# Performance work log

Hardware: AMD Instinct MI355X
Metric: run time of the kernel (lower is better)

## Reference

```python
import math
import jax, jax.numpy as jnp
import numpy as np

N_HEADS = 16
D_EMBED = 1024
D_HEAD = D_EMBED // N_HEADS
BATCH = 2
SEQ = 2048


def setup_inputs() -> dict:
    key = jax.random.key(0)
    k1, k2, k3 = jax.random.split(key, 3)
    scale = 1.0 / math.sqrt(D_EMBED)
    return {
        "x": jax.random.normal(k1, (1, BATCH, SEQ, D_EMBED), dtype=jnp.float32),
        "w_in": jax.random.normal(k2, (3 * D_EMBED, D_EMBED), dtype=jnp.float32) * scale,
        "b_in": jnp.zeros((3 * D_EMBED,), dtype=jnp.float32),
        "w_out": jax.random.normal(k3, (D_EMBED, D_EMBED), dtype=jnp.float32) * scale,
        "b_out": jnp.zeros((D_EMBED,), dtype=jnp.float32),
        "causal_mask": 1,
    }


def reference(x, w_in, b_in, w_out, b_out, causal_mask):
    lead, B, S, D = x.shape  # lead == 1
    H, dh = N_HEADS, D_HEAD
    # fused QKV projection (torch Linear: x @ W^T + b)
    qkv = jnp.einsum("lbsd,ed->lbse", x, w_in) + b_in
    q, k, v = jnp.split(qkv, 3, axis=-1)
    # [1,B,S,D] -> [B,H,S,dh]
    def to_heads(t):
        return t.reshape(B, S, H, dh).transpose(0, 2, 1, 3)
    q, k, v = to_heads(q), to_heads(k), to_heads(v)
    # scaled dot-product attention with optional causal mask
    scores = jnp.einsum("bhqd,bhkd->bhqk", q, k)
    if causal_mask:
        mask = jnp.triu(jnp.ones((S, S), dtype=bool), k=1)
        scores = jnp.where(mask, -jnp.inf, scores)
    scores = scores / math.sqrt(dh)
    attn = jax.nn.softmax(scores, axis=-1)
    out = jnp.einsum("bhqk,bhkd->bhqd", attn, v)
    out = out.transpose(0, 2, 1, 3).reshape(lead, B, S, D)
    return jnp.einsum("lbsd,ed->lbse", out, w_out) + b_out
```

## Files before the change

### kernel.cpp

```cpp
#include <hip/hip_runtime.h>
#include <hip/hip_bf16.h>
#include <stdint.h>

#define S_LEN 2048
#define D_EMB 1024
#define NHEAD 16
#define DHEAD 64
#define NBATCH 2
#define MROWS 4096

typedef __attribute__((ext_vector_type(8))) short bf16x8;
typedef __attribute__((ext_vector_type(4))) float f32x4;
typedef unsigned short u16;
typedef unsigned int u32;

__device__ __forceinline__ u16 f2bf(float f) {
  union { float f; u32 u; } v; v.f = f;
  u32 r = v.u + 0x7fffu + ((v.u >> 16) & 1u);
  return (u16)(r >> 16);
}

__device__ __forceinline__ void gl_lds16(const void* g, void* l) {
  __builtin_amdgcn_global_load_lds(
      (const __attribute__((address_space(1))) u32*)g,
      (__attribute__((address_space(3))) u32*)l, 16, 0, 0);
}

__device__ __forceinline__ int swz(int o) { return o ^ (((o >> 7) & 7) << 4); }

__global__ void cast_f32_bf16(const float* __restrict__ in, u16* __restrict__ out, int n4) {
  int i = blockIdx.x * blockDim.x + threadIdx.x;
  if (i < n4) {
    float4 v = reinterpret_cast<const float4*>(in)[i];
    ushort4 o;
    o.x = f2bf(v.x); o.y = f2bf(v.y); o.z = f2bf(v.z); o.w = f2bf(v.w);
    reinterpret_cast<ushort4*>(out)[i] = o;
  }
}

template <int EPI>
__launch_bounds__(256, 2)
__global__ void gemm_bt(const u16* __restrict__ A, const u16* __restrict__ Bm,
                        const float* __restrict__ bias, int M, int N, int K,
                        u16* __restrict__ q_out, u16* __restrict__ k_out,
                        u16* __restrict__ vt_out, float* __restrict__ f_out) {
  __shared__ __align__(16) u16 As[2][128 * 32];
  __shared__ __align__(16) u16 Bs[2][128 * 32];
  const int t = threadIdx.x;
  const int w = t >> 6, lane = t & 63;
  const int m0 = blockIdx.y * 128, n0 = blockIdx.x * 128;
  const int wr = w >> 1, wc = w & 1;

  f32x4 acc[4][4] = {};

  const int e0 = w * 512 + lane * 8;
  const int ar0 = e0 >> 5, ac0 = e0 & 31;
  const int e1 = e0 + 2048;
  const int ar1 = e1 >> 5, ac1 = e1 & 31;
  const u16* Ab0 = A + (size_t)(m0 + ar0) * K + ac0;
  const u16* Ab1 = A + (size_t)(m0 + ar1) * K + ac1;
  const u16* Bb0 = Bm + (size_t)(n0 + ar0) * K + ac0;
  const u16* Bb1 = Bm + (size_t)(n0 + ar1) * K + ac1;

  const int lr = lane & 15, lg = lane >> 4;

#define GSTAGE(KT, BUF)                                \
  do {                                                 \
    gl_lds16(Ab0 + (KT), &As[BUF][w * 512]);           \
    gl_lds16(Ab1 + (KT), &As[BUF][w * 512 + 2048]);    \
    gl_lds16(Bb0 + (KT), &Bs[BUF][w * 512]);           \
    gl_lds16(Bb1 + (KT), &Bs[BUF][w * 512 + 2048]);    \
  } while (0)

  GSTAGE(0, 0);
  __syncthreads();
  int cur = 0;
  for (int kt = 0; kt < K; kt += 32) {
    if (kt + 32 < K) GSTAGE(kt + 32, cur ^ 1);
    bf16x8 af[4], bfr[4];
#pragma unroll
    for (int i = 0; i < 4; i++)
      af[i] = *(const bf16x8*)&As[cur][(wr * 64 + i * 16 + lr) * 32 + lg * 8];
#pragma unroll
    for (int j = 0; j < 4; j++)
      bfr[j] = *(const bf16x8*)&Bs[cur][(wc * 64 + j * 16 + lr) * 32 + lg * 8];
#pragma unroll
    for (int i = 0; i < 4; i++)
#pragma unroll
      for (int j = 0; j < 4; j++)
        acc[i][j] = __builtin_amdgcn_mfma_f32_16x16x32_bf16(af[i], bfr[j], acc[i][j], 0, 0, 0);
    __syncthreads();
    cur ^= 1;
  }
#undef GSTAGE

#pragma unroll
  for (int j = 0; j < 4; j++) {
    const int n = n0 + wc * 64 + j * 16 + lr;
    const float bv = bias[n];
#pragma unroll
    for (int i = 0; i < 4; i++) {
#pragma unroll
      for (int r = 0; r < 4; r++) {
        const int m = m0 + wr * 64 + i * 16 + lg * 4 + r;
        float v = acc[i][j][r] + bv;
        if (EPI == 0) {
          const int which = n >> 10, nn = n & 1023;
          const int h = nn >> 6, d = nn & 63;
          const int b = m >> 11, s = m & 2047;
          if (which == 0)
            q_out[(size_t)(((b * NHEAD + h) * S_LEN) + s) * DHEAD + d] = f2bf(v * 0.125f);
          else if (which == 1)
            k_out[(size_t)(((b * NHEAD + h) * S_LEN) + s) * DHEAD + d] = f2bf(v);
          else
            vt_out[(size_t)(((b * NHEAD + h) * DHEAD) + d) * S_LEN + s] = f2bf(v);
        } else {
          f_out[(size_t)m * N + n] = v;
        }
      }
    }
  }
}

__launch_bounds__(512, 2)
__global__ void attn_kernel(const u16* __restrict__ Qg, const u16* __restrict__ Kg,
                            const u16* __restrict__ Vtg, u16* __restrict__ AO,
                            const int* __restrict__ causal) {
  __shared__ __align__(16) u16 Kt[2][64 * 64];
  __shared__ __align__(16) u16 Vt[2][64 * 64];
  __shared__ __align__(16) u16 Pl[8][16 * 72];

  const int t = threadIdx.x, w = t >> 6, lane = t & 63;
  const int lr = lane & 15, lg = lane >> 4;
  const int qt = (int)(gridDim.x - 1) - (int)blockIdx.x;
  const int bh = blockIdx.y;
  const size_t bh_off = (size_t)bh * S_LEN * DHEAD;
  const int cz = *causal;
  const int q0 = qt * 128;
  const int nk = cz ? (2 * qt + 2) : (S_LEN / 64);

  {
    const char* qb = (const char*)(Qg + bh_off + (size_t)q0 * DHEAD);
#pragma unroll
    for (int c = 0; c < 2; c++) {
      int drel = c * 8192 + w * 1024 + lane * 16;
      gl_lds16(qb + swz(drel), (char*)&Kt[0][0] + c * 8192 + w * 1024);
    }
  }
  __syncthreads();
  bf16x8 qf[2];
#pragma unroll
  for (int ks = 0; ks < 2; ks++) {
    int rq = w * 16 + lr;
    qf[ks] = *(const bf16x8*)((const char*)&Kt[0][0] + swz(rq * 128 + ks * 64 + lg * 16));
  }
  __syncthreads();

  auto stageK = [&](int kt, int buf) {
    const char* kb = (const char*)(Kg + bh_off + (size_t)kt * 64 * DHEAD);
    int drel = w * 1024 + lane * 16;
    gl_lds16(kb + swz(drel), (char*)&Kt[buf][0] + w * 1024);
  };
  auto stageV = [&](int kt, int buf) {
    int drel = w * 1024 + lane * 16;
    int o = swz(drel);
    int row = o >> 7, colb = o & 127;
    const char* vb = (const char*)Vtg +
                     (((size_t)bh * DHEAD + row) * S_LEN + (size_t)kt * 64) * 2 + colb;
    gl_lds16(vb, (char*)&Vt[buf][0] + w * 1024);
  };

  float m_run[4], l_run[4];
  f32x4 o_acc[4] = {};
#pragma unroll
  for (int r = 0; r < 4; r++) { m_run[r] = -INFINITY; l_run[r] = 0.f; }

  stageK(0, 0);
  stageV(0, 0);
  __syncthreads();
  int cur = 0;

  for (int kt = 0; kt < nk; kt++) {
    if (kt + 1 < nk) {
      stageK(kt + 1, cur ^ 1);
      stageV(kt + 1, cur ^ 1);
    }

    f32x4 s[4] = {};
#pragma unroll
    for (int nf = 0; nf < 4; nf++) {
#pragma unroll
      for (int ks = 0; ks < 2; ks++) {
        int r = nf * 16 + lr;
        bf16x8 kf = *(const bf16x8*)((const char*)&Kt[cur][0] + swz(r * 128 + ks * 64 + lg * 16));
        s[nf] = __builtin_amdgcn_mfma_f32_16x16x32_bf16(qf[ks], kf, s[nf], 0, 0, 0);
      }
    }

    if (cz && (kt * 64 + 63 > q0 + w * 16)) {
#pragma unroll
      for (int nf = 0; nf < 4; nf++)
#pragma unroll
        for (int r = 0; r < 4; r++) {
          int kv = kt * 64 + nf * 16 + lr;
          int qr = q0 + w * 16 + lg * 4 + r;
          if (kv > qr) s[nf][r] = -INFINITY;
        }
    }

    float rmax[4];
#pragma unroll
    for (int r = 0; r < 4; r++) {
      rmax[r] = s[0][r];
#pragma unroll
      for (int nf = 1; nf < 4; nf++) rmax[r] = fmaxf(rmax[r], s[nf][r]);
    }
#pragma unroll
    for (int mlt = 1; mlt < 16; mlt <<= 1)
#pragma unroll
      for (int r = 0; r < 4; r++) rmax[r] = fmaxf(rmax[r], __shfl_xor(rmax[r], mlt, 64));

    float scl[4];
#pragma unroll
    for (int r = 0; r < 4; r++) {
      float mn = fmaxf(m_run[r], rmax[r]);
      scl[r] = __expf(m_run[r] - mn);
      m_run[r] = mn;
    }

    float rsum[4] = {0.f, 0.f, 0.f, 0.f};
#pragma unroll
    for (int nf = 0; nf < 4; nf++)
#pragma unroll
      for (int r = 0; r < 4; r++) {
        float p = __expf(s[nf][r] - m_run[r]);
        rsum[r] += p;
        Pl[w][(lg * 4 + r) * 72 + nf * 16 + lr] = f2bf(p);
      }
#pragma unroll
    for (int mlt = 1; mlt < 16; mlt <<= 1)
#pragma unroll
      for (int r = 0; r < 4; r++) rsum[r] += __shfl_xor(rsum[r], mlt, 64);
#pragma unroll
    for (int r = 0; r < 4; r++) l_run[r] = l_run[r] * scl[r] + rsum[r];
#pragma unroll
    for (int nf = 0; nf < 4; nf++)
#pragma unroll
      for (int r = 0; r < 4; r++) o_acc[nf][r] *= scl[r];

    asm volatile("s_waitcnt lgkmcnt(0)" ::: "memory");
    __builtin_amdgcn_sched_barrier(0);

    bf16x8 pf[2];
#pragma unroll
    for (int ks = 0; ks < 2; ks++)
      pf[ks] = *(const bf16x8*)&Pl[w][lr * 72 + ks * 32 + lg * 8];
#pragma unroll
    for (int nf = 0; nf < 4; nf++) {
#pragma unroll
      for (int ks = 0; ks < 2; ks++) {
        int r = nf * 16 + lr;
        bf16x8 vf = *(const bf16x8*)((const char*)&Vt[cur][0] + swz(r * 128 + ks * 64 + lg * 16));
        o_acc[nf] = __builtin_amdgcn_mfma_f32_16x16x32_bf16(pf[ks], vf, o_acc[nf], 0, 0, 0);
      }
    }

    __syncthreads();
    cur ^= 1;
  }

  const int b = bh >> 4, h = bh & 15;
#pragma unroll
  for (int nf = 0; nf < 4; nf++)
#pragma unroll
    for (int r = 0; r < 4; r++) {
      float v = o_acc[nf][r] / l_run[r];
      int qrow = q0 + w * 16 + lg * 4 + r;
      int d = nf * 16 + lr;
      AO[(size_t)(b * S_LEN + qrow) * D_EMB + h * DHEAD + d] = f2bf(v);
    }
}

extern "C" void kernel_launch(void* const* d_in, const int* in_sizes, int n_in,
                              void* d_out, int out_size, void* d_ws, size_t ws_size,
                              hipStream_t stream) {
  const float* x = (const float*)d_in[0];
  const float* w_in = (const float*)d_in[1];
  const float* b_in = (const float*)d_in[2];
  const float* w_out = (const float*)d_in[3];
  const float* b_out = (const float*)d_in[4];
  const int* causal = (const int*)d_in[5];
  float* out = (float*)d_out;

  char* p = (char*)d_ws;
  u16* xb = (u16*)p;  p += (size_t)MROWS * D_EMB * 2;
  u16* wib = (u16*)p; p += (size_t)3 * D_EMB * D_EMB * 2;
  u16* wob = (u16*)p; p += (size_t)D_EMB * D_EMB * 2;
  u16* Qg = (u16*)p;  p += (size_t)MROWS * D_EMB * 2;
  u16* Kg = (u16*)p;  p += (size_t)MROWS * D_EMB * 2;
  u16* Vtg = (u16*)p; p += (size_t)MROWS * D_EMB * 2;
  u16* AO = (u16*)p;  p += (size_t)MROWS * D_EMB * 2;

  {
    int n4 = MROWS * D_EMB / 4;
    cast_f32_bf16<<<(n4 + 255) / 256, 256, 0, stream>>>(x, xb, n4);
  }
  {
    int n4 = 3 * D_EMB * D_EMB / 4;
    cast_f32_bf16<<<(n4 + 255) / 256, 256, 0, stream>>>(w_in, wib, n4);
  }
  {
    int n4 = D_EMB * D_EMB / 4;
    cast_f32_bf16<<<(n4 + 255) / 256, 256, 0, stream>>>(w_out, wob, n4);
  }

  gemm_bt<0><<<dim3(3 * D_EMB / 128, MROWS / 128), 256, 0, stream>>>(
      xb, wib, b_in, MROWS, 3 * D_EMB, D_EMB, Qg, Kg, Vtg, nullptr);

  attn_kernel<<<dim3(S_LEN / 128, NBATCH * NHEAD), 512, 0, stream>>>(Qg, Kg, Vtg, AO, causal);

  gemm_bt<1><<<dim3(D_EMB / 128, MROWS / 128), 256, 0, stream>>>(
      AO, wob, b_out, MROWS, D_EMB, D_EMB, nullptr, nullptr, nullptr, out);
}
```

Before: 252.0 us.

## Use exp2 softmax with lazy max rescaling and MFMA row sums

Folds log2(e) into the Q scale so the softmax can use exp2f. The running max is now updated only when some row's tile max exceeds it by more than a threshold, which skips the cross-lane max reduction and rescaling in most iterations. Row sums come from an MFMA against a ones vector on the bf16 P, replacing the shuffle-based sum reduction. The q-tile order is also reversed for half of the heads to balance causal work. The trade-off is that P can grow up to 2^8 before rounding to bf16, and the row sums now use the rounded bf16 values.

```diff
diff --git a/kernel.cpp b/kernel.cpp
--- a/kernel.cpp
+++ b/kernel.cpp
@@ -109,7 +109,7 @@
           const int h = nn >> 6, d = nn & 63;
           const int b = m >> 11, s = m & 2047;
           if (which == 0)
-            q_out[(size_t)(((b * NHEAD + h) * S_LEN) + s) * DHEAD + d] = f2bf(v * 0.125f);
+            q_out[(size_t)(((b * NHEAD + h) * S_LEN) + s) * DHEAD + d] = f2bf(v * 0.180336880f);
           else if (which == 1)
             k_out[(size_t)(((b * NHEAD + h) * S_LEN) + s) * DHEAD + d] = f2bf(v);
           else
@@ -132,12 +132,17 @@
 
   const int t = threadIdx.x, w = t >> 6, lane = t & 63;
   const int lr = lane & 15, lg = lane >> 4;
-  const int qt = (int)(gridDim.x - 1) - (int)blockIdx.x;
+  const int nqt = (int)gridDim.x;
+  const int qt = ((int)blockIdx.y < 16) ? (nqt - 1 - (int)blockIdx.x) : (int)blockIdx.x;
   const int bh = blockIdx.y;
   const size_t bh_off = (size_t)bh * S_LEN * DHEAD;
   const int cz = *causal;
   const int q0 = qt * 128;
   const int nk = cz ? (2 * qt + 2) : (S_LEN / 64);
+
+  bf16x8 ones;
+#pragma unroll
+  for (int e = 0; e < 8; e++) ones[e] = (short)16256;
 
   {
     const char* qb = (const char*)(Qg + bh_off + (size_t)q0 * DHEAD);
@@ -208,45 +213,38 @@
         }
     }
 
-    float rmax[4];
-#pragma unroll
-    for (int r = 0; r < 4; r++) {
-      rmax[r] = s[0][r];
-#pragma unroll
-      for (int nf = 1; nf < 4; nf++) rmax[r] = fmaxf(rmax[r], s[nf][r]);
-    }
-#pragma unroll
-    for (int mlt = 1; mlt < 16; mlt <<= 1)
-#pragma unroll
-      for (int r = 0; r < 4; r++) rmax[r] = fmaxf(rmax[r], __shfl_xor(rmax[r], mlt, 64));
-
-    float scl[4];
-#pragma unroll
-    for (int r = 0; r < 4; r++) {
-      float mn = fmaxf(m_run[r], rmax[r]);
-      scl[r] = __expf(m_run[r] - mn);
-      m_run[r] = mn;
-    }
-
-    float rsum[4] = {0.f, 0.f, 0.f, 0.f};
+    float lmax[4];
+#pragma unroll
+    for (int r = 0; r < 4; r++)
+      lmax[r] = fmaxf(fmaxf(s[0][r], s[1][r]), fmaxf(s[2][r], s[3][r]));
+    float need = fmaxf(fmaxf(lmax[0] - m_run[0], lmax[1] - m_run[1]),
+                       fmaxf(lmax[2] - m_run[2], lmax[3] - m_run[3]));
+    if (!__all(need <= 8.0f)) {
+      float rmax[4];
+#pragma unroll
+      for (int r = 0; r < 4; r++) rmax[r] = lmax[r];
+#pragma unroll
+      for (int mlt = 1; mlt < 16; mlt <<= 1)
+#pragma unroll
+        for (int r = 0; r < 4; r++) rmax[r] = fmaxf(rmax[r], __shfl_xor(rmax[r], mlt, 64));
+#pragma unroll
+      for (int r = 0; r < 4; r++) {
+        float mn = fmaxf(m_run[r], rmax[r]);
+        float scl = exp2f(m_run[r] - mn);
+        m_run[r] = mn;
+        l_run[r] *= scl;
+#pragma unroll
+        for (int nf = 0; nf < 4; nf++) o_acc[nf][r] *= scl;
+      }
+    }
+
 #pragma unroll
     for (int nf = 0; nf < 4; nf++)
 #pragma unroll
       for (int r = 0; r < 4; r++) {
-        float p = __expf(s[nf][r] - m_run[r]);
-        rsum[r] += p;
+        float p = exp2f(s[nf][r] - m_run[r]);
         Pl[w][(lg * 4 + r) * 72 + nf * 16 + lr] = f2bf(p);
       }
-#pragma unroll
-    for (int mlt = 1; mlt < 16; mlt <<= 1)
-#pragma unroll
-      for (int r = 0; r < 4; r++) rsum[r] += __shfl_xor(rsum[r], mlt, 64);
-#pragma unroll
-    for (int r = 0; r < 4; r++) l_run[r] = l_run[r] * scl[r] + rsum[r];
-#pragma unroll
-    for (int nf = 0; nf < 4; nf++)
-#pragma unroll
-      for (int r = 0; r < 4; r++) o_acc[nf][r] *= scl[r];
 
     asm volatile("s_waitcnt lgkmcnt(0)" ::: "memory");
     __builtin_amdgcn_sched_barrier(0);
@@ -255,6 +253,11 @@
 #pragma unroll
     for (int ks = 0; ks < 2; ks++)
       pf[ks] = *(const bf16x8*)&Pl[w][lr * 72 + ks * 32 + lg * 8];
+
+    f32x4 lsum = {};
+    lsum = __builtin_amdgcn_mfma_f32_16x16x32_bf16(pf[0], ones, lsum, 0, 0, 0);
+    lsum = __builtin_amdgcn_mfma_f32_16x16x32_bf16(pf[1], ones, lsum, 0, 0, 0);
+
 #pragma unroll
     for (int nf = 0; nf < 4; nf++) {
 #pragma unroll
@@ -264,6 +267,8 @@
         o_acc[nf] = __builtin_amdgcn_mfma_f32_16x16x32_bf16(pf[ks], vf, o_acc[nf], 0, 0, 0);
       }
     }
+#pragma unroll
+    for (int r = 0; r < 4; r++) l_run[r] += lsum[r];
 
     __syncthreads();
     cur ^= 1;
```

Result: faster. 206.6 us (-18.0%).
